# Kernel tuning notes

Measured on AMD Instinct MI355X. Metric: run time of the kernel, lower is better.

Reference implementation:

```python
import jax, jax.numpy as jnp
import numpy as np

D, M, R, N = 64, 256, 3, 1024
L_MID = 2  # number of middle phi layers (L=4 total)


def sp10(x):
    # torch.nn.Softplus(beta=10)
    return jax.nn.softplus(10.0 * x) / 10.0


def setup_inputs() -> dict:
    key = jax.random.key(0)
    ks = jax.random.split(key, 16)
    w_scale = 1.0 / np.sqrt(R)
    a_ht_scale = 0.1 / np.sqrt(M)
    inp = {
        "X": jax.random.uniform(ks[0], (N, D), dtype=jnp.float32),
        "w_first": 1.0 * jax.random.normal(ks[1], (D, M, 1, R), dtype=jnp.float32),
        "w_mid": w_scale * jax.random.normal(ks[2], (L_MID, D, M, R, R), dtype=jnp.float32),
        "w_last": w_scale * jax.random.normal(ks[3], (D, M, R, 1), dtype=jnp.float32),
        "b_first": 0.1 * jax.random.normal(ks[4], (D, M, R), dtype=jnp.float32),
        "b_mid": 0.1 * jax.random.normal(ks[5], (L_MID, D, M, R), dtype=jnp.float32),
        "b_last": 0.1 * jax.random.normal(ks[6], (D, M, 1), dtype=jnp.float32),
        "a_first": jax.random.normal(ks[7], (D, M, R), dtype=jnp.float32),
        "a_mid": jax.random.normal(ks[8], (L_MID, D, M, R), dtype=jnp.float32),
    }
    # HT mixing matrices: init m*eye(m) per group (as in source) + small noise
    dims = [32, 16, 8, 4, 2]
    for i, g in enumerate(dims):
        eye = M * jnp.eye(M, dtype=jnp.float32)
        inp[f"aHT{i}"] = jnp.tile(eye[None], (g, 1, 1)) + 0.01 * jax.random.normal(ks[9 + i], (g, M, M), dtype=jnp.float32)
    inp["aHT5"] = a_ht_scale * jax.random.normal(ks[15], (1, M, 1), dtype=jnp.float32)
    return inp


def _layer(phis, phidots, w, b, a):
    # one hidden layer of the per-(d,m) rank-r MLP chain
    W = sp10(w)                                            # (d,m,k,l) >= 0
    z = jnp.einsum('ndmk,dmkl->ndml', phis, W) + b         # affine
    tz = jnp.tanh(z)
    ta = jnp.tanh(a)
    phidots = jnp.einsum('ndmk,dmkl->ndml', phidots, W) * (1.0 + ta * (1.0 - tz * tz))
    phis = z + tz * ta
    return phis, phidots


def _forward(X, w_first, w_mid, w_last, b_first, b_mid, b_last, a_first, a_mid,
             aHT0, aHT1, aHT2, aHT3, aHT4, aHT5):
    n = X.shape[0]
    phis = jnp.broadcast_to(X[:, :, None, None], (n, D, M, 1))  # expand_X
    phidots = jnp.ones_like(phis)
    phis, phidots = _layer(phis, phidots, w_first, b_first, a_first)
    for i in range(w_mid.shape[0]):
        phis, phidots = _layer(phis, phidots, w_mid[i], b_mid[i], a_mid[i])
    Wl = sp10(w_last)
    z = jnp.einsum('ndmk,dmkl->ndml', phis, Wl) + b_last   # (n,d,m,1)
    s = jax.nn.sigmoid(z)
    phidots = (jnp.einsum('ndmk,dmkl->ndml', phidots, Wl) * (s * (1.0 - s)))[..., 0]  # (n,d,m)
    # HT contraction: default couplings = consecutive pairs, d=64 -> 6 levels
    T = phidots
    for a in (aHT0, aHT1, aHT2, aHT3, aHT4, aHT5):
        nn_, dim, m_ = T.shape
        T = T.reshape(nn_, dim // 2, 2, m_).prod(axis=2)   # product over each pair
        A = sp10(a)
        A = A / A.sum(axis=1, keepdims=True)               # column-normalized nonneg mix
        T = jnp.einsum('ngm,gmk->ngk', T, A)
    return T[:, 0, 0]                                      # likelihood, shape (n,)


def reference(X, w_first, w_mid, w_last, b_first, b_mid, b_last, a_first, a_mid,
              aHT0, aHT1, aHT2, aHT3, aHT4, aHT5):
    return _forward(X, w_first, w_mid, w_last, b_first, b_mid, b_last,
                    a_first, a_mid, aHT0, aHT1, aHT2, aHT3, aHT4, aHT5)
```

## Files before the change

### kernel.cpp

```cpp
#include <hip/hip_runtime.h>
#include <cstdint>
#include <cstddef>

#define D_DIM 64
#define M_DIM 256
#define N_PTS 1024

typedef __attribute__((ext_vector_type(4))) float f32x4;
typedef __attribute__((ext_vector_type(2))) float f32x2;
typedef __attribute__((ext_vector_type(8))) short s16x8;

static __device__ __forceinline__ f32x2 pkfma(f32x2 a, f32x2 b, f32x2 c) {
#if __has_builtin(__builtin_elementwise_fma)
    return __builtin_elementwise_fma(a, b, c);
#else
    f32x2 r; r.x = fmaf(a.x, b.x, c.x); r.y = fmaf(a.y, b.y, c.y); return r;
#endif
}
static __device__ __forceinline__ f32x2 sp2(float s) {
    f32x2 r; r.x = s; r.y = s; return r;
}

static __device__ __forceinline__ float sp10f(float x) {
    float t = 10.f * x;
    return 0.1f * (fmaxf(t, 0.f) + log1pf(__expf(-fabsf(t))));
}

static __device__ __forceinline__ f32x2 ftanh2(f32x2 x) {
    f32x2 xs = x * sp2(2.88539008177793f);
    f32x2 e;
    e.x = __builtin_amdgcn_exp2f(xs.x);
    e.y = __builtin_amdgcn_exp2f(xs.y);
    f32x2 ep = e + sp2(1.f);
    f32x2 r;
    r.x = __builtin_amdgcn_rcpf(ep.x);
    r.y = __builtin_amdgcn_rcpf(ep.y);
    return pkfma(sp2(-2.f), r, sp2(1.f));
}

static __device__ __forceinline__ unsigned short f2bf(float x) {
    unsigned u = __float_as_uint(x);
    u = u + 0x7FFFu + ((u >> 16) & 1u);
    return (unsigned short)(u >> 16);
}
static __device__ __forceinline__ float bf2f(unsigned short h) {
    return __uint_as_float(((unsigned)h) << 16);
}

static __device__ __forceinline__ void split1(float x, unsigned& uh, unsigned& ul) {
    unsigned u = __float_as_uint(x);
    uh = u + 0x7FFFu + ((u >> 16) & 1u);
    ul = __float_as_uint(x - __uint_as_float(uh & 0xFFFF0000u));
}

static __device__ __forceinline__ const float* map_g(int g, const float* a0, const float* a1,
                                                     const float* a2, const float* a3,
                                                     const float* a4, int& lg) {
    if (g < 32) { lg = g;      return a0; }
    if (g < 48) { lg = g - 32; return a1; }
    if (g < 56) { lg = g - 48; return a2; }
    if (g < 60) { lg = g - 56; return a3; }
    lg = g - 60; return a4;
}

__global__ __launch_bounds__(256) void k_prep3(
    const float* __restrict__ X, const float* __restrict__ wf,
    const float* __restrict__ wm, const float* __restrict__ wl,
    const float* __restrict__ b1, const float* __restrict__ bm,
    const float* __restrict__ bl, const float* __restrict__ af,
    const float* __restrict__ am,
    const float* __restrict__ a0, const float* __restrict__ a1,
    const float* __restrict__ a2, const float* __restrict__ a3,
    const float* __restrict__ a4,
    float* __restrict__ Wpack, float* __restrict__ Xt,
    unsigned short* __restrict__ Anth, unsigned short* __restrict__ Antl) {
    __shared__ float tile[64][65];
    const int t = threadIdx.x;
    const int b = blockIdx.x;
    if (b < 16) {
        const int n0 = b * 64;
#pragma unroll
        for (int i = 0; i < 4; i++) {
            const int f   = i * 256 + t;
            const int row = f >> 4;
            const int c4  = f & 15;
            float4 v = *(const float4*)(X + (size_t)(n0 + row) * 64 + c4 * 4);
            tile[row][c4 * 4 + 0] = v.x;
            tile[row][c4 * 4 + 1] = v.y;
            tile[row][c4 * 4 + 2] = v.z;
            tile[row][c4 * 4 + 3] = v.w;
        }
        __syncthreads();
#pragma unroll
        for (int i = 0; i < 4; i++) {
            const int f    = i * 256 + t;
            const int drow = f >> 4;
            const int c4   = f & 15;
            float4 v;
            v.x = tile[c4 * 4 + 0][drow];
            v.y = tile[c4 * 4 + 1][drow];
            v.z = tile[c4 * 4 + 2][drow];
            v.w = tile[c4 * 4 + 3][drow];
            *(float4*)(Xt + (size_t)drow * 1024 + n0 + c4 * 4) = v;
        }
        return;
    }
    if (b < 80) {
        const int id = (b - 16) * 256 + t;
        float r[48];
#pragma unroll
        for (int q = 0; q < 48; q++) r[q] = 0.f;
#pragma unroll
        for (int q = 0; q < 3; q++) {
            r[0 + q] = sp10f(wf[id * 3 + q]);
            r[3 + q] = b1[id * 3 + q];
            r[6 + q] = tanhf(af[id * 3 + q]);
            r[39 + q] = sp10f(wl[id * 3 + q]);
        }
#pragma unroll
        for (int l = 0; l < 2; l++) {
            const size_t b9 = ((size_t)l * 16384 + id) * 9;
            const size_t b3 = ((size_t)l * 16384 + id) * 3;
#pragma unroll
            for (int q = 0; q < 9; q++) r[9 + l * 15 + q] = sp10f(wm[b9 + q]);
#pragma unroll
            for (int q = 0; q < 3; q++) {
                r[18 + l * 15 + q] = bm[b3 + q];
                r[21 + l * 15 + q] = tanhf(am[b3 + q]);
            }
        }
        r[42] = bl[id];
        float4* o = (float4*)(Wpack + (size_t)id * 48);
#pragma unroll
        for (int q = 0; q < 12; q++) o[q] = ((float4*)r)[q];
        return;
    }
    const int idx = b - 80;
    const int g   = idx >> 4;
    const int rr  = idx & 15;
    const int m0  = (rr & 3) * 64;
    const int k0  = (rr >> 2) * 64;
    int lg;
    const float* A  = map_g(g, a0, a1, a2, a3, a4, lg);
    const float* Ag = A + (size_t)lg * 65536;

#pragma unroll
    for (int i = 0; i < 4; i++) {
        const int f   = i * 256 + t;
        const int row = f >> 4;
        const int c4  = f & 15;
        float4 v = *(const float4*)(Ag + (size_t)(m0 + row) * 256 + k0 + c4 * 4);
        tile[row][c4 * 4 + 0] = v.x;
        tile[row][c4 * 4 + 1] = v.y;
        tile[row][c4 * 4 + 2] = v.z;
        tile[row][c4 * 4 + 3] = v.w;
    }
    __syncthreads();

#pragma unroll
    for (int i = 0; i < 4; i++) {
        const int f    = i * 256 + t;
        const int krow = f >> 4;
        const int c4   = f & 15;
        float v0 = sp10f(tile[c4 * 4 + 0][krow]);
        float v1 = sp10f(tile[c4 * 4 + 1][krow]);
        float v2 = sp10f(tile[c4 * 4 + 2][krow]);
        float v3 = sp10f(tile[c4 * 4 + 3][krow]);
        unsigned short h0 = f2bf(v0), h1 = f2bf(v1), h2 = f2bf(v2), h3 = f2bf(v3);
        ushort4 hi, lo;
        hi.x = h0; hi.y = h1; hi.z = h2; hi.w = h3;
        lo.x = f2bf(v0 - bf2f(h0));
        lo.y = f2bf(v1 - bf2f(h1));
        lo.z = f2bf(v2 - bf2f(h2));
        lo.w = f2bf(v3 - bf2f(h3));
        const size_t dst = (size_t)g * 65536 + (size_t)(k0 + krow) * 256 + m0 + c4 * 4;
        *(ushort4*)(Anth + dst) = hi;
        *(ushort4*)(Antl + dst) = lo;
    }
}

__global__ void k_csum_t(const unsigned short* __restrict__ Anth,
                         const unsigned short* __restrict__ Antl,
                         float* __restrict__ csum) {
    const int g    = blockIdx.x;
    const int w    = threadIdx.x >> 6;
    const int lane = threadIdx.x & 63;
    const int k    = blockIdx.y * 4 + w;
    const size_t base = (size_t)g * 65536 + k * 256 + lane * 4;
    uint2 vh = *(const uint2*)(Anth + base);
    uint2 vl = *(const uint2*)(Antl + base);
    float s = 0.f;
    s += bf2f((unsigned short)(vh.x & 0xFFFFu)) + bf2f((unsigned short)(vh.x >> 16));
    s += bf2f((unsigned short)(vh.y & 0xFFFFu)) + bf2f((unsigned short)(vh.y >> 16));
    s += bf2f((unsigned short)(vl.x & 0xFFFFu)) + bf2f((unsigned short)(vl.x >> 16));
    s += bf2f((unsigned short)(vl.y & 0xFFFFu)) + bf2f((unsigned short)(vl.y >> 16));
    for (int off = 32; off > 0; off >>= 1) s += __shfl_down(s, off);
    if (lane == 0) csum[g * 256 + k] = s;
}

__global__ __launch_bounds__(512, 1) void k_phase1(
    const float* __restrict__ Xt, const float* __restrict__ Wpack,
    unsigned short* __restrict__ P0h, unsigned short* __restrict__ P0l) {
    __shared__ float sT[128][33];
    __shared__ float sXd[2][128];
    const int j  = blockIdx.x;
    const int mc = blockIdx.y;
    const int n0 = blockIdx.z * 128;
    const int t  = threadIdx.x;
    const int w    = __builtin_amdgcn_readfirstlane(t >> 6);
    const int lane = t & 63;

    if (t < 256)
        sXd[t >> 7][t & 127] = Xt[(size_t)(2 * j + (t >> 7)) * 1024 + n0 + (t & 127)];
    __syncthreads();

    f32x2 xe0, xe1;
    xe0.x = sXd[0][lane]; xe0.y = sXd[0][64 + lane];
    xe1.x = sXd[1][lane]; xe1.y = sXd[1][64 + lane];

    const f32x2 one2 = sp2(1.f);
    f32x2 p0;

#pragma unroll 2
    for (int it = 0; it < 8; it++) {
        const int i  = it >> 1;
        const int e  = it & 1;
        const int mm = w * 4 + i;
        const int m  = mc * 32 + mm;
        const float* __restrict__ rp =
            Wpack + (size_t)(((2 * j + e) << 8) + m) * 48;
        float W1a[3], B1a[3], T1a[3], Wm[2][9], Bm[2][3], Tm[2][3], Wla[3];
#pragma unroll
        for (int r = 0; r < 3; r++) {
            W1a[r] = rp[r];
            B1a[r] = rp[3 + r];
            T1a[r] = rp[6 + r];
            Bm[0][r] = rp[18 + r];
            Tm[0][r] = rp[21 + r];
            Bm[1][r] = rp[33 + r];
            Tm[1][r] = rp[36 + r];
            Wla[r] = rp[39 + r];
        }
#pragma unroll
        for (int q = 0; q < 9; q++) {
            Wm[0][q] = rp[9 + q];
            Wm[1][q] = rp[24 + q];
        }
        const float Bla = rp[42];

        const f32x2 x = e ? xe1 : xe0;
        f32x2 phi[3], pd[3];
#pragma unroll
        for (int r = 0; r < 3; r++) {
            f32x2 z  = pkfma(x, sp2(W1a[r]), sp2(B1a[r]));
            f32x2 tz = ftanh2(z);
            f32x2 ta = sp2(T1a[r]);
            pd[r]  = sp2(W1a[r]) * pkfma(ta, pkfma(-tz, tz, one2), one2);
            phi[r] = pkfma(tz, ta, z);
        }
#pragma unroll
        for (int l = 0; l < 2; l++) {
            f32x2 nphi[3], npd[3];
#pragma unroll
            for (int q = 0; q < 3; q++) {
                f32x2 z  = sp2(Bm[l][q]);
                f32x2 dp = sp2(0.f);
#pragma unroll
                for (int r = 0; r < 3; r++) {
                    f32x2 wv = sp2(Wm[l][r * 3 + q]);
                    z  = pkfma(phi[r], wv, z);
                    dp = pkfma(pd[r],  wv, dp);
                }
                f32x2 tz = ftanh2(z);
                f32x2 ta = sp2(Tm[l][q]);
                nphi[q] = pkfma(tz, ta, z);
                npd[q]  = dp * pkfma(ta, pkfma(-tz, tz, one2), one2);
            }
#pragma unroll
            for (int q = 0; q < 3; q++) { phi[q] = nphi[q]; pd[q] = npd[q]; }
        }
        f32x2 z  = sp2(Bla);
        f32x2 dp = sp2(0.f);
#pragma unroll
        for (int r = 0; r < 3; r++) {
            f32x2 wv = sp2(Wla[r]);
            z  = pkfma(phi[r], wv, z);
            dp = pkfma(pd[r],  wv, dp);
        }
        f32x2 zs = z * sp2(-1.4426950408889634f);
        f32x2 s;
        s.x = __builtin_amdgcn_rcpf(1.f + __builtin_amdgcn_exp2f(zs.x));
        s.y = __builtin_amdgcn_rcpf(1.f + __builtin_amdgcn_exp2f(zs.y));
        f32x2 prod = dp * s * (one2 - s);
        if (e == 0) {
            p0 = prod;
        } else {
            sT[lane][mm]      = p0.x * prod.x;
            sT[64 + lane][mm] = p0.y * prod.y;
        }
    }
    __syncthreads();

    const size_t base = ((size_t)j * N_PTS + n0) * M_DIM + mc * 32;
#pragma unroll
    for (int it = 0; it < 2; it++) {
        const int idx = it * 512 + t;
        const int row = idx >> 3;
        const int c4  = idx & 7;
        float4 v;
        v.x = sT[row][c4 * 4 + 0];
        v.y = sT[row][c4 * 4 + 1];
        v.z = sT[row][c4 * 4 + 2];
        v.w = sT[row][c4 * 4 + 3];
        unsigned uh0, ul0, uh1, ul1, uh2, ul2, uh3, ul3;
        split1(v.x, uh0, ul0);
        split1(v.y, uh1, ul1);
        split1(v.z, uh2, ul2);
        split1(v.w, uh3, ul3);
        uint2 hp, lp;
        hp.x = __builtin_amdgcn_perm(uh1, uh0, 0x07060302u);
        hp.y = __builtin_amdgcn_perm(uh3, uh2, 0x07060302u);
        lp.x = __builtin_amdgcn_perm(ul1, ul0, 0x07060302u);
        lp.y = __builtin_amdgcn_perm(ul3, ul2, 0x07060302u);
        *(uint2*)(P0h + base + (size_t)row * M_DIM + c4 * 4) = hp;
        *(uint2*)(P0l + base + (size_t)row * M_DIM + c4 * 4) = lp;
    }
}

#define LDST64 72

__global__ __launch_bounds__(256, 4) void k_g64ps(
    const unsigned short* __restrict__ Th, const unsigned short* __restrict__ Tl,
    const unsigned short* __restrict__ Bh, const unsigned short* __restrict__ Bl,
    const float* __restrict__ csum, float* __restrict__ Tout) {
    __shared__ unsigned short sAh[64 * LDST64];
    __shared__ unsigned short sAl[64 * LDST64];
    __shared__ unsigned short sBh[64 * LDST64];
    __shared__ unsigned short sBl[64 * LDST64];

    const int g  = blockIdx.z;
    const int n0 = blockIdx.x * 64;
    const int k0 = blockIdx.y * 64;
    const unsigned short* Thg = Th + (size_t)g * N_PTS * 256;
    const unsigned short* Tlg = Tl + (size_t)g * N_PTS * 256;
    const unsigned short* Bhg = Bh + (size_t)g * 65536;
    const unsigned short* Blg = Bl + (size_t)g * 65536;

    const int tid  = threadIdx.x;
    const int lane = tid & 63;
    const int w    = tid >> 6;
    const int wr   = w >> 1;
    const int wc   = w & 1;
    const int lr   = lane & 15;
    const int lk   = lane >> 4;

    f32x4 acc[2][2];
#pragma unroll
    for (int a = 0; a < 2; a++)
#pragma unroll
        for (int b = 0; b < 2; b++) acc[a][b] = (f32x4){0.f, 0.f, 0.f, 0.f};

    for (int kb = 0; kb < 256; kb += 64) {
#pragma unroll
        for (int i = 0; i < 2; i++) {
            const int idx = i * 256 + tid;
            const int row = idx >> 3;
            const int seg = idx & 7;
            const size_t srcA = (size_t)(n0 + row) * 256 + kb + seg * 8;
            const size_t srcB = (size_t)(k0 + row) * 256 + kb + seg * 8;
            *(uint4*)&sAh[row * LDST64 + seg * 8] = *(const uint4*)(Thg + srcA);
            *(uint4*)&sAl[row * LDST64 + seg * 8] = *(const uint4*)(Tlg + srcA);
            *(uint4*)&sBh[row * LDST64 + seg * 8] = *(const uint4*)(Bhg + srcB);
            *(uint4*)&sBl[row * LDST64 + seg * 8] = *(const uint4*)(Blg + srcB);
        }
        __syncthreads();

        s16x8 ah[2][2], al[2][2], bh[2][2], bl[2][2];
#pragma unroll
        for (int nt = 0; nt < 2; nt++)
#pragma unroll
            for (int ks = 0; ks < 2; ks++) {
                const int off = (wr * 32 + nt * 16 + lr) * LDST64 + ks * 32 + lk * 8;
                ah[nt][ks] = *(const s16x8*)&sAh[off];
                al[nt][ks] = *(const s16x8*)&sAl[off];
            }
#pragma unroll
        for (int kt = 0; kt < 2; kt++)
#pragma unroll
            for (int ks = 0; ks < 2; ks++) {
                const int off = (wc * 32 + kt * 16 + lr) * LDST64 + ks * 32 + lk * 8;
                bh[kt][ks] = *(const s16x8*)&sBh[off];
                bl[kt][ks] = *(const s16x8*)&sBl[off];
            }
#pragma unroll
        for (int ks = 0; ks < 2; ks++)
#pragma unroll
            for (int nt = 0; nt < 2; nt++)
#pragma unroll
                for (int kt = 0; kt < 2; kt++) {
                    acc[nt][kt] = __builtin_amdgcn_mfma_f32_16x16x32_bf16(ah[nt][ks], bh[kt][ks], acc[nt][kt], 0, 0, 0);
                    acc[nt][kt] = __builtin_amdgcn_mfma_f32_16x16x32_bf16(ah[nt][ks], bl[kt][ks], acc[nt][kt], 0, 0, 0);
                    acc[nt][kt] = __builtin_amdgcn_mfma_f32_16x16x32_bf16(al[nt][ks], bh[kt][ks], acc[nt][kt], 0, 0, 0);
                }
        __syncthreads();
    }

    float* Og = Tout + (size_t)g * N_PTS * 256;
#pragma unroll
    for (int kt = 0; kt < 2; kt++) {
        const int col = k0 + wc * 32 + kt * 16 + lr;
        const float inv = 1.0f / csum[g * 256 + col];
#pragma unroll
        for (int nt = 0; nt < 2; nt++) {
            const int rbase = n0 + wr * 32 + nt * 16 + lk * 4;
#pragma unroll
            for (int r = 0; r < 4; r++)
                Og[(size_t)(rbase + r) * 256 + col] = acc[nt][kt][r] * inv;
        }
    }
}

__global__ __launch_bounds__(256, 4) void k_gemm64(const float* __restrict__ Tin,
                                                   const unsigned short* __restrict__ Bh,
                                                   const unsigned short* __restrict__ Bl,
                                                   const float* __restrict__ csum,
                                                   float* __restrict__ Tout) {
    __shared__ unsigned short sAh[64 * LDST64];
    __shared__ unsigned short sAl[64 * LDST64];
    __shared__ unsigned short sBh[64 * LDST64];
    __shared__ unsigned short sBl[64 * LDST64];

    const int g  = blockIdx.z;
    const int n0 = blockIdx.x * 64;
    const int k0 = blockIdx.y * 64;
    const float* T0  = Tin + (size_t)(2 * g) * N_PTS * 256;
    const float* T1p = T0 + (size_t)N_PTS * 256;
    const unsigned short* Bhg = Bh + (size_t)g * 65536;
    const unsigned short* Blg = Bl + (size_t)g * 65536;

    const int tid  = threadIdx.x;
    const int lane = tid & 63;
    const int w    = tid >> 6;
    const int wr   = w >> 1;
    const int wc   = w & 1;
    const int lr   = lane & 15;
    const int lk   = lane >> 4;

    f32x4 acc[2][2];
#pragma unroll
    for (int a = 0; a < 2; a++)
#pragma unroll
        for (int b = 0; b < 2; b++) acc[a][b] = (f32x4){0.f, 0.f, 0.f, 0.f};

    for (int kb = 0; kb < 256; kb += 64) {
#pragma unroll
        for (int i = 0; i < 4; i++) {
            const int idx = i * 256 + tid;
            const int row = idx >> 4;
            const int c4  = idx & 15;
            float4 v = *(const float4*)(T0 + (size_t)(n0 + row) * 256 + kb + c4 * 4);
            float4 u = *(const float4*)(T1p + (size_t)(n0 + row) * 256 + kb + c4 * 4);
            v.x *= u.x; v.y *= u.y; v.z *= u.z; v.w *= u.w;
            unsigned uh0, ul0, uh1, ul1, uh2, ul2, uh3, ul3;
            split1(v.x, uh0, ul0);
            split1(v.y, uh1, ul1);
            split1(v.z, uh2, ul2);
            split1(v.w, uh3, ul3);
            uint2 hp, lp;
            hp.x = __builtin_amdgcn_perm(uh1, uh0, 0x07060302u);
            hp.y = __builtin_amdgcn_perm(uh3, uh2, 0x07060302u);
            lp.x = __builtin_amdgcn_perm(ul1, ul0, 0x07060302u);
            lp.y = __builtin_amdgcn_perm(ul3, ul2, 0x07060302u);
            *(uint2*)&sAh[row * LDST64 + c4 * 4] = hp;
            *(uint2*)&sAl[row * LDST64 + c4 * 4] = lp;
        }
#pragma unroll
        for (int i = 0; i < 2; i++) {
            const int idx = i * 256 + tid;
            const int row = idx >> 3;
            const int seg = idx & 7;
            const size_t src = (size_t)(k0 + row) * 256 + kb + seg * 8;
            *(uint4*)&sBh[row * LDST64 + seg * 8] = *(const uint4*)(Bhg + src);
            *(uint4*)&sBl[row * LDST64 + seg * 8] = *(const uint4*)(Blg + src);
        }
        __syncthreads();

        s16x8 ah[2][2], al[2][2], bh[2][2], bl[2][2];
#pragma unroll
        for (int nt = 0; nt < 2; nt++)
#pragma unroll
            for (int ks = 0; ks < 2; ks++) {
                const int off = (wr * 32 + nt * 16 + lr) * LDST64 + ks * 32 + lk * 8;
                ah[nt][ks] = *(const s16x8*)&sAh[off];
                al[nt][ks] = *(const s16x8*)&sAl[off];
            }
#pragma unroll
        for (int kt = 0; kt < 2; kt++)
#pragma unroll
            for (int ks = 0; ks < 2; ks++) {
                const int off = (wc * 32 + kt * 16 + lr) * LDST64 + ks * 32 + lk * 8;
                bh[kt][ks] = *(const s16x8*)&sBh[off];
                bl[kt][ks] = *(const s16x8*)&sBl[off];
            }
#pragma unroll
        for (int ks = 0; ks < 2; ks++)
#pragma unroll
            for (int nt = 0; nt < 2; nt++)
#pragma unroll
                for (int kt = 0; kt < 2; kt++) {
                    acc[nt][kt] = __builtin_amdgcn_mfma_f32_16x16x32_bf16(ah[nt][ks], bh[kt][ks], acc[nt][kt], 0, 0, 0);
                    acc[nt][kt] = __builtin_amdgcn_mfma_f32_16x16x32_bf16(ah[nt][ks], bl[kt][ks], acc[nt][kt], 0, 0, 0);
                    acc[nt][kt] = __builtin_amdgcn_mfma_f32_16x16x32_bf16(al[nt][ks], bh[kt][ks], acc[nt][kt], 0, 0, 0);
                }
        __syncthreads();
    }

    float* Og = Tout + (size_t)g * N_PTS * 256;
#pragma unroll
    for (int kt = 0; kt < 2; kt++) {
        const int col = k0 + wc * 32 + kt * 16 + lr;
        const float inv = 1.0f / csum[g * 256 + col];
#pragma unroll
        for (int nt = 0; nt < 2; nt++) {
            const int rbase = n0 + wr * 32 + nt * 16 + lk * 4;
#pragma unroll
            for (int r = 0; r < 4; r++)
                Og[(size_t)(rbase + r) * 256 + col] = acc[nt][kt][r] * inv;
        }
    }
}

__global__ void k_l5(const float* __restrict__ Tin, const float* __restrict__ a5,
                     float* __restrict__ out) {
    const int n = blockIdx.x;
    const int m = threadIdx.x;
    __shared__ float sv[256], sw[256];
    float w = sp10f(a5[m]);
    float v = Tin[(size_t)n * 256 + m] * Tin[(size_t)(N_PTS + n) * 256 + m] * w;
    sv[m] = v;
    sw[m] = w;
    __syncthreads();
    for (int s = 128; s > 0; s >>= 1) {
        if (m < s) { sv[m] += sv[m + s]; sw[m] += sw[m + s]; }
        __syncthreads();
    }
    if (m == 0) out[n] = sv[0] / sw[0];
}

extern "C" void kernel_launch(void* const* d_in, const int* in_sizes, int n_in,
                              void* d_out, int out_size, void* d_ws, size_t ws_size,
                              hipStream_t stream) {
    const float* X  = (const float*)d_in[0];
    const float* wf = (const float*)d_in[1];
    const float* wm = (const float*)d_in[2];
    const float* wl = (const float*)d_in[3];
    const float* b1 = (const float*)d_in[4];
    const float* bm = (const float*)d_in[5];
    const float* bl = (const float*)d_in[6];
    const float* af = (const float*)d_in[7];
    const float* am = (const float*)d_in[8];
    const float* a0 = (const float*)d_in[9];
    const float* a1 = (const float*)d_in[10];
    const float* a2 = (const float*)d_in[11];
    const float* a3 = (const float*)d_in[12];
    const float* a4 = (const float*)d_in[13];
    const float* a5 = (const float*)d_in[14];
    float* out = (float*)d_out;

    float* ws    = (float*)d_ws;
    float* Wpack = ws;
    float* Xt    = Wpack + 786432;
    float* csum  = Xt + 65536;
    unsigned short* Anth = (unsigned short*)(csum + 15872);
    unsigned short* Antl = Anth + (size_t)62 * 65536;
    float* B0    = (float*)(Antl + (size_t)62 * 65536);
    float* B1    = B0 + (size_t)32 * N_PTS * M_DIM;
    unsigned short* P0h = (unsigned short*)B1;
    unsigned short* P0l = P0h + (size_t)32 * N_PTS * M_DIM;

    k_prep3<<<1072, 256, 0, stream>>>(X, wf, wm, wl, b1, bm, bl, af, am,
                                      a0, a1, a2, a3, a4, Wpack, Xt, Anth, Antl);
    k_csum_t<<<dim3(62, 64), 256, 0, stream>>>(Anth, Antl, csum);
    k_phase1<<<dim3(32, 8, 8), 512, 0, stream>>>(Xt, Wpack, P0h, P0l);

    k_g64ps<<<dim3(16, 4, 32), 256, 0, stream>>>(P0h, P0l, Anth, Antl, csum, B0);
    k_gemm64<<<dim3(16, 4, 16), 256, 0, stream>>>(B0, Anth + (size_t)32 * 65536,
                                                  Antl + (size_t)32 * 65536, csum + 32 * 256, B1);
    k_gemm64<<<dim3(16, 4, 8), 256, 0, stream>>>(B1, Anth + (size_t)48 * 65536,
                                                 Antl + (size_t)48 * 65536, csum + 48 * 256, B0);
    k_gemm64<<<dim3(16, 4, 4), 256, 0, stream>>>(B0, Anth + (size_t)56 * 65536,
                                                 Antl + (size_t)56 * 65536, csum + 56 * 256, B1);
    k_gemm64<<<dim3(16, 4, 2), 256, 0, stream>>>(B1, Anth + (size_t)60 * 65536,
                                                 Antl + (size_t)60 * 65536, csum + 60 * 256, B0);
    k_l5<<<N_PTS, 256, 0, stream>>>(B0, a5, out);
}
```

Before: 145.6 us.

## Split pairwise product and bf16 split into separate kernel before each HT GEMM

The fused k_gemm64, which multiplied pairs of fp32 tiles and split them into bf16 hi/lo inside every GEMM block, is removed. A standalone k_pair kernel now computes the pairwise product and hi/lo split once per element, and the pre-split k_g64ps GEMM is reused for all HT levels. This removes redundant pair-multiply and split work, since each element was previously reprocessed by every column block (4x). In exchange it adds four extra kernel launches and an extra write and read of the split buffers through global memory.

```diff
diff --git a/kernel.cpp b/kernel.cpp
--- a/kernel.cpp
+++ b/kernel.cpp
@@ -327,6 +327,34 @@
     }
 }
 
+__global__ __launch_bounds__(256) void k_pair(const float* __restrict__ G,
+                                              unsigned short* __restrict__ Qh,
+                                              unsigned short* __restrict__ Ql) {
+    const int i = blockIdx.x * 256 + threadIdx.x;
+#pragma unroll
+    for (int s = 0; s < 2; s++) {
+        const int idx = i * 2 + s;
+        const int q = idx >> 16;
+        const int r = idx & 65535;
+        const float4 a = *(const float4*)(G + ((size_t)(2 * q) << 18) + r * 4);
+        const float4 b = *(const float4*)(G + ((size_t)(2 * q + 1) << 18) + r * 4);
+        float4 v;
+        v.x = a.x * b.x; v.y = a.y * b.y; v.z = a.z * b.z; v.w = a.w * b.w;
+        unsigned uh0, ul0, uh1, ul1, uh2, ul2, uh3, ul3;
+        split1(v.x, uh0, ul0);
+        split1(v.y, uh1, ul1);
+        split1(v.z, uh2, ul2);
+        split1(v.w, uh3, ul3);
+        uint2 hp, lp;
+        hp.x = __builtin_amdgcn_perm(uh1, uh0, 0x07060302u);
+        hp.y = __builtin_amdgcn_perm(uh3, uh2, 0x07060302u);
+        lp.x = __builtin_amdgcn_perm(ul1, ul0, 0x07060302u);
+        lp.y = __builtin_amdgcn_perm(ul3, ul2, 0x07060302u);
+        *(uint2*)(Qh + ((size_t)q << 18) + r * 4) = hp;
+        *(uint2*)(Ql + ((size_t)q << 18) + r * 4) = lp;
+    }
+}
+
 #define LDST64 72
 
 __global__ __launch_bounds__(256, 4) void k_g64ps(
@@ -341,10 +369,10 @@
     const int g  = blockIdx.z;
     const int n0 = blockIdx.x * 64;
     const int k0 = blockIdx.y * 64;
-    const unsigned short* Thg = Th + (size_t)g * N_PTS * 256;
-    const unsigned short* Tlg = Tl + (size_t)g * N_PTS * 256;
-    const unsigned short* Bhg = Bh + (size_t)g * 65536;
-    const unsigned short* Blg = Bl + (size_t)g * 65536;
+    const unsigned short* Thg = Th + ((size_t)g << 18);
+    const unsigned short* Tlg = Tl + ((size_t)g << 18);
+    const unsigned short* Bhg = Bh + ((size_t)g << 16);
+    const unsigned short* Blg = Bl + ((size_t)g << 16);
 
     const int tid  = threadIdx.x;
     const int lane = tid & 63;
@@ -405,117 +433,7 @@
         __syncthreads();
     }
 
-    float* Og = Tout + (size_t)g * N_PTS * 256;
-#pragma unroll
-    for (int kt = 0; kt < 2; kt++) {
-        const int col = k0 + wc * 32 + kt * 16 + lr;
-        const float inv = 1.0f / csum[g * 256 + col];
-#pragma unroll
-        for (int nt = 0; nt < 2; nt++) {
-            const int rbase = n0 + wr * 32 + nt * 16 + lk * 4;
-#pragma unroll
-            for (int r = 0; r < 4; r++)
-                Og[(size_t)(rbase + r) * 256 + col] = acc[nt][kt][r] * inv;
-        }
-    }
-}
-
-__global__ __launch_bounds__(256, 4) void k_gemm64(const float* __restrict__ Tin,
-                                                   const unsigned short* __restrict__ Bh,
-                                                   const unsigned short* __restrict__ Bl,
-                                                   const float* __restrict__ csum,
-                                                   float* __restrict__ Tout) {
-    __shared__ unsigned short sAh[64 * LDST64];
-    __shared__ unsigned short sAl[64 * LDST64];
-    __shared__ unsigned short sBh[64 * LDST64];
-    __shared__ unsigned short sBl[64 * LDST64];
-
-    const int g  = blockIdx.z;
-    const int n0 = blockIdx.x * 64;
-    const int k0 = blockIdx.y * 64;
-    const float* T0  = Tin + (size_t)(2 * g) * N_PTS * 256;
-    const float* T1p = T0 + (size_t)N_PTS * 256;
-    const unsigned short* Bhg = Bh + (size_t)g * 65536;
-    const unsigned short* Blg = Bl + (size_t)g * 65536;
-
-    const int tid  = threadIdx.x;
-    const int lane = tid & 63;
-    const int w    = tid >> 6;
-    const int wr   = w >> 1;
-    const int wc   = w & 1;
-    const int lr   = lane & 15;
-    const int lk   = lane >> 4;
-
-    f32x4 acc[2][2];
-#pragma unroll
-    for (int a = 0; a < 2; a++)
-#pragma unroll
-        for (int b = 0; b < 2; b++) acc[a][b] = (f32x4){0.f, 0.f, 0.f, 0.f};
-
-    for (int kb = 0; kb < 256; kb += 64) {
-#pragma unroll
-        for (int i = 0; i < 4; i++) {
-            const int idx = i * 256 + tid;
-            const int row = idx >> 4;
-            const int c4  = idx & 15;
-            float4 v = *(const float4*)(T0 + (size_t)(n0 + row) * 256 + kb + c4 * 4);
-            float4 u = *(const float4*)(T1p + (size_t)(n0 + row) * 256 + kb + c4 * 4);
-            v.x *= u.x; v.y *= u.y; v.z *= u.z; v.w *= u.w;
-            unsigned uh0, ul0, uh1, ul1, uh2, ul2, uh3, ul3;
-            split1(v.x, uh0, ul0);
-            split1(v.y, uh1, ul1);
-            split1(v.z, uh2, ul2);
-            split1(v.w, uh3, ul3);
-            uint2 hp, lp;
-            hp.x = __builtin_amdgcn_perm(uh1, uh0, 0x07060302u);
-            hp.y = __builtin_amdgcn_perm(uh3, uh2, 0x07060302u);
-            lp.x = __builtin_amdgcn_perm(ul1, ul0, 0x07060302u);
-            lp.y = __builtin_amdgcn_perm(ul3, ul2, 0x07060302u);
-            *(uint2*)&sAh[row * LDST64 + c4 * 4] = hp;
-            *(uint2*)&sAl[row * LDST64 + c4 * 4] = lp;
-        }
-#pragma unroll
-        for (int i = 0; i < 2; i++) {
-            const int idx = i * 256 + tid;
-            const int row = idx >> 3;
-            const int seg = idx & 7;
-            const size_t src = (size_t)(k0 + row) * 256 + kb + seg * 8;
-            *(uint4*)&sBh[row * LDST64 + seg * 8] = *(const uint4*)(Bhg + src);
-            *(uint4*)&sBl[row * LDST64 + seg * 8] = *(const uint4*)(Blg + src);
-        }
-        __syncthreads();
-
-        s16x8 ah[2][2], al[2][2], bh[2][2], bl[2][2];
-#pragma unroll
-        for (int nt = 0; nt < 2; nt++)
-#pragma unroll
-            for (int ks = 0; ks < 2; ks++) {
-                const int off = (wr * 32 + nt * 16 + lr) * LDST64 + ks * 32 + lk * 8;
-                ah[nt][ks] = *(const s16x8*)&sAh[off];
-                al[nt][ks] = *(const s16x8*)&sAl[off];
-            }
-#pragma unroll
-        for (int kt = 0; kt < 2; kt++)
-#pragma unroll
-            for (int ks = 0; ks < 2; ks++) {
-                const int off = (wc * 32 + kt * 16 + lr) * LDST64 + ks * 32 + lk * 8;
-                bh[kt][ks] = *(const s16x8*)&sBh[off];
-                bl[kt][ks] = *(const s16x8*)&sBl[off];
-            }
-#pragma unroll
-        for (int ks = 0; ks < 2; ks++)
-#pragma unroll
-            for (int nt = 0; nt < 2; nt++)
-#pragma unroll
-                for (int kt = 0; kt < 2; kt++) {
-                    acc[nt][kt] = __builtin_amdgcn_mfma_f32_16x16x32_bf16(ah[nt][ks], bh[kt][ks], acc[nt][kt], 0, 0, 0);
-                    acc[nt][kt] = __builtin_amdgcn_mfma_f32_16x16x32_bf16(ah[nt][ks], bl[kt][ks], acc[nt][kt], 0, 0, 0);
-                    acc[nt][kt] = __builtin_amdgcn_mfma_f32_16x16x32_bf16(al[nt][ks], bh[kt][ks], acc[nt][kt], 0, 0, 0);
-                }
-        __syncthreads();
-    }
-
-    float* Og = Tout + (size_t)g * N_PTS * 256;
+    float* Og = Tout + ((size_t)g << 18);
 #pragma unroll
     for (int kt = 0; kt < 2; kt++) {
         const int col = k0 + wc * 32 + kt * 16 + lr;
@@ -573,24 +491,33 @@
     float* csum  = Xt + 65536;
     unsigned short* Anth = (unsigned short*)(csum + 15872);
     unsigned short* Antl = Anth + (size_t)62 * 65536;
-    float* B0    = (float*)(Antl + (size_t)62 * 65536);
-    float* B1    = B0 + (size_t)32 * N_PTS * M_DIM;
-    unsigned short* P0h = (unsigned short*)B1;
-    unsigned short* P0l = P0h + (size_t)32 * N_PTS * M_DIM;
+    unsigned short* P0h  = Antl + (size_t)62 * 65536;
+    unsigned short* P0l  = P0h + (size_t)32 * 262144;
+    float* Gbuf  = (float*)(P0l + (size_t)32 * 262144);
+    unsigned short* Qh   = (unsigned short*)(Gbuf + (size_t)32 * 262144);
+    unsigned short* Ql   = Qh + (size_t)16 * 262144;
 
     k_prep3<<<1072, 256, 0, stream>>>(X, wf, wm, wl, b1, bm, bl, af, am,
                                       a0, a1, a2, a3, a4, Wpack, Xt, Anth, Antl);
     k_csum_t<<<dim3(62, 64), 256, 0, stream>>>(Anth, Antl, csum);
     k_phase1<<<dim3(32, 8, 8), 512, 0, stream>>>(Xt, Wpack, P0h, P0l);
 
-    k_g64ps<<<dim3(16, 4, 32), 256, 0, stream>>>(P0h, P0l, Anth, Antl, csum, B0);
-    k_gemm64<<<dim3(16, 4, 16), 256, 0, stream>>>(B0, Anth + (size_t)32 * 65536,
-                                                  Antl + (size_t)32 * 65536, csum + 32 * 256, B1);
-    k_gemm64<<<dim3(16, 4, 8), 256, 0, stream>>>(B1, Anth + (size_t)48 * 65536,
-                                                 Antl + (size_t)48 * 65536, csum + 48 * 256, B0);
-    k_gemm64<<<dim3(16, 4, 4), 256, 0, stream>>>(B0, Anth + (size_t)56 * 65536,
-                                                 Antl + (size_t)56 * 65536, csum + 56 * 256, B1);
-    k_gemm64<<<dim3(16, 4, 2), 256, 0, stream>>>(B1, Anth + (size_t)60 * 65536,
-                                                 Antl + (size_t)60 * 65536, csum + 60 * 256, B0);
-    k_l5<<<N_PTS, 256, 0, stream>>>(B0, a5, out);
-}
+    k_g64ps<<<dim3(16, 4, 32), 256, 0, stream>>>(P0h, P0l, Anth, Antl, csum, Gbuf);
+    k_pair<<<2048, 256, 0, stream>>>(Gbuf, Qh, Ql);
+    k_g64ps<<<dim3(16, 4, 16), 256, 0, stream>>>(Qh, Ql, Anth + (size_t)32 * 65536,
+                                                 Antl + (size_t)32 * 65536,
+                                                 csum + 32 * 256, Gbuf);
+    k_pair<<<1024, 256, 0, stream>>>(Gbuf, Qh, Ql);
+    k_g64ps<<<dim3(16, 4, 8), 256, 0, stream>>>(Qh, Ql, Anth + (size_t)48 * 65536,
+                                                Antl + (size_t)48 * 65536,
+                                                csum + 48 * 256, Gbuf);
+    k_pair<<<512, 256, 0, stream>>>(Gbuf, Qh, Ql);
+    k_g64ps<<<dim3(16, 4, 4), 256, 0, stream>>>(Qh, Ql, Anth + (size_t)56 * 65536,
+                                                Antl + (size_t)56 * 65536,
+                                                csum + 56 * 256, Gbuf);
+    k_pair<<<256, 256, 0, stream>>>(Gbuf, Qh, Ql);
+    k_g64ps<<<dim3(16, 4, 2), 256, 0, stream>>>(Qh, Ql, Anth + (size_t)60 * 65536,
+                                                Antl + (size_t)60 * 65536,
+                                                csum + 60 * 256, Gbuf);
+    k_l5<<<N_PTS, 256, 0, stream>>>(Gbuf, a5, out);
+}
```

Result: slower. 162.6 us (median of 2 runs) (+11.7%).
